# Kernel tuning notes

Measured on AMD Instinct MI355X. Metric: run time of the kernel, lower is better.

## Reference

```python
import jax, jax.numpy as jnp
import numpy as np

N = 100000   # nodes
E = 1600000  # edges
F_IN = 4
H = 64
G = 1000     # graphs in batch
C = 3        # num_classes
L = 2        # num_unit (LEConv layers)


def setup_inputs() -> dict:
    key = jax.random.key(0)
    ks = jax.random.split(key, 14)
    s = 0.1
    return {
        "x": jax.random.normal(ks[0], (N, F_IN), jnp.float32),
        "edge_index": jax.random.randint(ks[1], (2, E), 0, N, dtype=jnp.int32),
        "edge_attr": jax.random.uniform(ks[2], (E,), jnp.float32),
        "batch": jnp.sort(jax.random.randint(ks[3], (N,), 0, G, dtype=jnp.int32)),
        "w_emb": jax.random.normal(ks[4], (F_IN, H), jnp.float32) * s,
        "b_emb": jnp.zeros((H,), jnp.float32),
        "lin1_w": jax.random.normal(ks[5], (L, H, H), jnp.float32) * s,
        "lin1_b": jnp.zeros((L, H), jnp.float32),
        "lin2_w": jax.random.normal(ks[6], (L, H, H), jnp.float32) * s,  # bias=False in PyG LEConv
        "lin3_w": jax.random.normal(ks[7], (L, H, H), jnp.float32) * s,
        "lin3_b": jnp.zeros((L, H), jnp.float32),
        "mlp_w1": jax.random.normal(ks[8], (H, 2 * H), jnp.float32) * s,
        "mlp_b1": jnp.zeros((2 * H,), jnp.float32),
        "mlp_w2": jax.random.normal(ks[9], (2 * H, C), jnp.float32) * s,
        "mlp_b2": jnp.zeros((C,), jnp.float32),
    }


def reference(x, edge_index, edge_attr, batch, w_emb, b_emb,
              lin1_w, lin1_b, lin2_w, lin3_w, lin3_b,
              mlp_w1, mlp_b1, mlp_w2, mlp_b2):
    src, dst = edge_index[0], edge_index[1]  # message flows src(j) -> dst(i)
    h = x @ w_emb + b_emb  # [N, H]
    for l in range(L):
        a = h @ lin1_w[l] + lin1_b[l]            # lin1(x_j) source side
        b = h @ lin2_w[l]                         # lin2(x_i) target side, no bias
        msg = (a[src] - b[dst]) * edge_attr[:, None]   # [E, H]
        agg = jax.ops.segment_sum(msg, dst, num_segments=N)
        h = jax.nn.relu(agg + h @ lin3_w[l] + lin3_b[l])
    # global_mean_pool
    sums = jax.ops.segment_sum(h, batch, num_segments=G)        # [G, H]
    counts = jax.ops.segment_sum(jnp.ones((N,), h.dtype), batch, num_segments=G)
    graph_x = sums / jnp.maximum(counts, 1.0)[:, None]
    # causal_mlp head
    return jax.nn.relu(graph_x @ mlp_w1 + mlp_b1) @ mlp_w2 + mlp_b2  # [G, C]
```

## Files before the change

### kernel.cpp

```cpp
#include <hip/hip_runtime.h>

#define N_NODES 100000
#define N_EDGES 1600000
#define F_INPUT 4
#define HDIM 64
#define G_GRAPHS 1000
#define C_CLS 3

#define NPB 256
#define BSHIFT 8
#define NB 391
#define CBLK 98
#define CSR_CAP 6144
#define HIST_BLOCKS 512
#define BNDS_BLOCKS 391

typedef __attribute__((ext_vector_type(8))) short bf16x8;
typedef __attribute__((ext_vector_type(4))) float f32x4;

__device__ __forceinline__ unsigned short f2bf(float f) {
    unsigned u = __float_as_uint(f);
    unsigned r = (u + 0x7FFF + ((u >> 16) & 1)) >> 16;
    return (unsigned short)r;
}
__device__ __forceinline__ float bflo(unsigned u) {
    return __uint_as_float(u << 16);
}
__device__ __forceinline__ float bfhi(unsigned u) {
    return __uint_as_float(u & 0xFFFF0000u);
}
__device__ __forceinline__ float bf1(unsigned short s) {
    return __uint_as_float(((unsigned)s) << 16);
}

__global__ __launch_bounds__(256) void k_prew(
    const float* __restrict__ w_emb, const float* __restrict__ b_emb,
    const float* __restrict__ lin1_w, const float* __restrict__ lin1_b,
    const float* __restrict__ lin2_w,
    const float* __restrict__ lin3_w, const float* __restrict__ lin3_b,
    float* __restrict__ wp, float* __restrict__ bp, int* __restrict__ bcnt) {
    int t = threadIdx.x;
    for (int i = t; i < NB; i += 256) bcnt[i] = 0;
    int k = t >> 6, f = t & 63;
    const float* Ws[3] = {lin1_w, lin2_w, lin3_w};
#pragma unroll
    for (int m = 0; m < 3; ++m) {
        float s = 0.f;
        for (int j = 0; j < HDIM; ++j) s += w_emb[k * HDIM + j] * Ws[m][j * HDIM + f];
        wp[m * 256 + k * HDIM + f] = s;
    }
    if (t < HDIM) {
#pragma unroll
        for (int m = 0; m < 3; ++m) {
            float s = 0.f;
            for (int j = 0; j < HDIM; ++j) s += b_emb[j] * Ws[m][j * HDIM + t];
            if (m == 0) s += lin1_b[t];
            if (m == 2) s += lin3_b[t];
            bp[m * HDIM + t] = s;
        }
    }
}

__global__ __launch_bounds__(256) void k_hist_bounds(
    const int* __restrict__ dst, int* __restrict__ bcnt,
    const int* __restrict__ batch, int* __restrict__ goff) {
    __shared__ int s[NB];
    if (blockIdx.x < HIST_BLOCKS) {
        int bb = blockIdx.x;
        for (int i = threadIdx.x; i < NB; i += 256) s[i] = 0;
        __syncthreads();
        const int4* dst4 = (const int4*)dst;
        for (int e4 = bb * 256 + threadIdx.x; e4 < N_EDGES / 4; e4 += HIST_BLOCKS * 256) {
            int4 d = dst4[e4];
            atomicAdd(&s[d.x >> BSHIFT], 1);
            atomicAdd(&s[d.y >> BSHIFT], 1);
            atomicAdd(&s[d.z >> BSHIFT], 1);
            atomicAdd(&s[d.w >> BSHIFT], 1);
        }
        __syncthreads();
        for (int i = threadIdx.x; i < NB; i += 256)
            if (s[i]) atomicAdd(&bcnt[i], s[i]);
    } else {
        int n = (blockIdx.x - HIST_BLOCKS) * 256 + threadIdx.x;
        if (n >= N_NODES) return;
        int bv = batch[n];
        int bp_ = (n == 0) ? -1 : batch[n - 1];
        for (int g = bp_ + 1; g <= bv; ++g) goff[g] = n;
        if (n == N_NODES - 1) {
            for (int g = bv + 1; g <= G_GRAPHS; ++g) goff[g] = N_NODES;
        }
    }
}

__global__ __launch_bounds__(512) void k_boff(
    const int* __restrict__ bcnt, int* __restrict__ boff, int* __restrict__ bcur) {
    __shared__ int s[512];
    int t = threadIdx.x;
    int v = (t < NB) ? bcnt[t] : 0;
    s[t] = v;
    __syncthreads();
    for (int d = 1; d < 512; d <<= 1) {
        int x2 = (t >= d) ? s[t - d] : 0;
        __syncthreads();
        s[t] += x2;
        __syncthreads();
    }
    int ex = s[t] - v;
    if (t < NB) { boff[t] = ex; bcur[t] = ex; }
    if (t == 0) boff[NB] = N_EDGES;
}

__global__ __launch_bounds__(1024) void k_bucket(const int* __restrict__ src,
                                                 const int* __restrict__ dst,
                                                 const float* __restrict__ attr,
                                                 int* __restrict__ bcur,
                                                 int2* __restrict__ bbuf) {
    __shared__ int cnt[NB];
    __shared__ int base[NB];
    for (int i = threadIdx.x; i < NB; i += 1024) cnt[i] = 0;
    __syncthreads();
    int e0 = blockIdx.x * 16384;
    int myb[16], myrank[16];
    int2 mypack[16];
#pragma unroll
    for (int k = 0; k < 16; ++k) {
        int e = e0 + k * 1024 + threadIdx.x;
        if (e < N_EDGES) {
            int d = dst[e];
            int b = d >> BSHIFT;
            myb[k] = b;
            myrank[k] = atomicAdd(&cnt[b], 1);
            mypack[k].x = src[e] | ((d & (NPB - 1)) << 17);
            mypack[k].y = __float_as_int(attr[e]);
        } else
            myb[k] = -1;
    }
    __syncthreads();
    for (int i = threadIdx.x; i < NB; i += 1024)
        base[i] = cnt[i] ? atomicAdd(&bcur[i], cnt[i]) : 0;
    __syncthreads();
#pragma unroll
    for (int k = 0; k < 16; ++k)
        if (myb[k] >= 0) bbuf[base[myb[k]] + myrank[k]] = mypack[k];
}

__global__ __launch_bounds__(256) void k_csr(const int2* __restrict__ bbuf,
                                             const int* __restrict__ boff,
                                             int* __restrict__ off,
                                             float* __restrict__ wsum,
                                             int2* __restrict__ edge2) {
    __shared__ int2 se[CSR_CAP];
    __shared__ int deg[NPB];
    __shared__ float wsm[NPB];
    __shared__ int loff[NPB];
    __shared__ int sct[256];
    int b = blockIdx.x;
    int lo = boff[b];
    int cnt = boff[b + 1] - lo;
    if (cnt > CSR_CAP) cnt = CSR_CAP;
    int t = threadIdx.x;
    deg[t] = 0;
    wsm[t] = 0.f;
    for (int i = t; i < cnt; i += 256) se[i] = bbuf[lo + i];
    __syncthreads();
    for (int i = t; i < cnt; i += 256) {
        int2 p = se[i];
        int dloc = (p.x >> 17) & (NPB - 1);
        atomicAdd(&deg[dloc], 1);
        atomicAdd(&wsm[dloc], __int_as_float(p.y));
    }
    __syncthreads();
    int v = deg[t];
    sct[t] = v;
    __syncthreads();
    for (int d = 1; d < 256; d <<= 1) {
        int x2 = (t >= d) ? sct[t - d] : 0;
        __syncthreads();
        sct[t] += x2;
        __syncthreads();
    }
    int ex = sct[t] - v;
    loff[t] = ex;
    __syncthreads();
    int n = b * NPB + t;
    if (n < N_NODES) { off[n] = lo + ex; wsum[n] = wsm[t]; }
    if (b == NB - 1 && t == 0) off[N_NODES] = N_EDGES;
    deg[t] = 0;
    __syncthreads();
    for (int i = t; i < cnt; i += 256) {
        int2 p = se[i];
        int dloc = (p.x >> 17) & (NPB - 1);
        int r = atomicAdd(&deg[dloc], 1);
        edge2[lo + loff[dloc] + r] = make_int2(p.x & 0x1FFFF, p.y);
    }
}

__global__ __launch_bounds__(256) void k_gemm1st(
    const float* __restrict__ x, const float* __restrict__ wp,
    const float* __restrict__ bp, const float* __restrict__ wsum,
    unsigned short* __restrict__ a_out, unsigned short* __restrict__ d_out_) {
    int wave = threadIdx.x >> 6;
    int lane = threadIdx.x & 63;
    int row = lane & 15;
    int kg = lane >> 4;
    int base = blockIdx.x * 64;
    int col = wave * 16 + row;

    bf16x8 Bf[3];
#pragma unroll
    for (int m = 0; m < 3; ++m) {
        union { bf16x8 v; unsigned short u[8]; } fr;
#pragma unroll
        for (int j = 0; j < 8; ++j)
            fr.u[j] = (kg == 0 && j < F_INPUT) ? f2bf(wp[m * 256 + j * HDIM + col])
                                               : (unsigned short)0;
        Bf[m] = fr.v;
    }
    float bias1 = bp[col], bias2 = bp[HDIM + col], bias3 = bp[2 * HDIM + col];

    f32x4 acc[3][4];
#pragma unroll
    for (int m = 0; m < 3; ++m)
#pragma unroll
        for (int t = 0; t < 4; ++t) acc[m][t] = (f32x4){0.f, 0.f, 0.f, 0.f};

#pragma unroll
    for (int t = 0; t < 4; ++t) {
        int n = base + t * 16 + row;
        union { bf16x8 v; unsigned short u[8]; } af;
#pragma unroll
        for (int j = 0; j < 8; ++j) af.u[j] = 0;
        if (kg == 0 && n < N_NODES) {
            float4 xv = *(const float4*)(x + (size_t)n * F_INPUT);
            af.u[0] = f2bf(xv.x); af.u[1] = f2bf(xv.y);
            af.u[2] = f2bf(xv.z); af.u[3] = f2bf(xv.w);
        }
#pragma unroll
        for (int m = 0; m < 3; ++m)
            acc[m][t] = __builtin_amdgcn_mfma_f32_16x16x32_bf16(af.v, Bf[m], acc[m][t], 0, 0, 0);
    }

#pragma unroll
    for (int t = 0; t < 4; ++t) {
#pragma unroll
        for (int r = 0; r < 4; ++r) {
            int n = base + t * 16 + kg * 4 + r;
            if (n >= N_NODES) continue;
            float ws = wsum[n];
            float av = acc[0][t][r] + bias1;
            float dv = acc[2][t][r] + bias3 - (acc[1][t][r] + bias2) * ws;
            a_out[(size_t)n * HDIM + col] = f2bf(av);
            d_out_[(size_t)n * HDIM + col] = f2bf(dv);
        }
    }
}

__global__ __launch_bounds__(256) void k_gemm3(
    const unsigned short* __restrict__ h,
    const float* __restrict__ W1, const float* __restrict__ b1,
    const float* __restrict__ W2,
    const float* __restrict__ W3, const float* __restrict__ b3,
    const float* __restrict__ wsum,
    unsigned short* __restrict__ a_out, unsigned short* __restrict__ d_out_) {
    int wave = threadIdx.x >> 6;
    int lane = threadIdx.x & 63;
    int row = lane & 15;
    int kg = lane >> 4;
    int base = blockIdx.x * 64;
    int col = wave * 16 + row;

    bf16x8 Bf[3][2];
    const float* Ws[3] = {W1, W2, W3};
#pragma unroll
    for (int m = 0; m < 3; ++m)
#pragma unroll
        for (int hf = 0; hf < 2; ++hf) {
            union { bf16x8 v; unsigned short u[8]; } fr;
#pragma unroll
            for (int j = 0; j < 8; ++j) {
                int k = hf * 32 + kg * 8 + j;
                fr.u[j] = f2bf(Ws[m][k * HDIM + col]);
            }
            Bf[m][hf] = fr.v;
        }

    float bias1 = b1[col];
    float bias3 = b3[col];

    f32x4 acc[3][4];
#pragma unroll
    for (int m = 0; m < 3; ++m)
#pragma unroll
        for (int t = 0; t < 4; ++t) acc[m][t] = (f32x4){0.f, 0.f, 0.f, 0.f};

#pragma unroll
    for (int t = 0; t < 4; ++t) {
        int n = base + t * 16 + row;
        bf16x8 a0, a1;
        if (n < N_NODES) {
            const unsigned short* hr = h + (size_t)n * HDIM;
            a0 = *(const bf16x8*)(hr + kg * 8);
            a1 = *(const bf16x8*)(hr + 32 + kg * 8);
        } else {
            a0 = (bf16x8){0,0,0,0,0,0,0,0};
            a1 = (bf16x8){0,0,0,0,0,0,0,0};
        }
#pragma unroll
        for (int m = 0; m < 3; ++m) {
            acc[m][t] = __builtin_amdgcn_mfma_f32_16x16x32_bf16(a0, Bf[m][0], acc[m][t], 0, 0, 0);
            acc[m][t] = __builtin_amdgcn_mfma_f32_16x16x32_bf16(a1, Bf[m][1], acc[m][t], 0, 0, 0);
        }
    }

#pragma unroll
    for (int t = 0; t < 4; ++t) {
#pragma unroll
        for (int r = 0; r < 4; ++r) {
            int n = base + t * 16 + kg * 4 + r;
            if (n >= N_NODES) continue;
            float ws = wsum[n];
            float av = acc[0][t][r] + bias1;
            float dv = acc[2][t][r] + bias3 - acc[1][t][r] * ws;
            a_out[(size_t)n * HDIM + col] = f2bf(av);
            d_out_[(size_t)n * HDIM + col] = f2bf(dv);
        }
    }
}

__global__ __launch_bounds__(256) void k_agg(const int2* __restrict__ edge2,
                                             const int* __restrict__ off,
                                             const unsigned short* __restrict__ a,
                                             const unsigned short* __restrict__ dbuf,
                                             unsigned short* __restrict__ h) {
    int wid = threadIdx.x >> 6;
    int lane = threadIdx.x & 63;
    int slot = lane >> 3;
    int fo = lane & 7;
    int n = blockIdx.x * 4 + wid;
    if (n >= N_NODES) return;
    int lo = off[n], hi = off[n + 1];

    float acc[8];
#pragma unroll
    for (int q = 0; q < 8; ++q) acc[q] = 0.f;

#define GATHER_ADD(J)                                                        \
    if ((J) < hi) {                                                          \
        int2 p = edge2[(J)];                                                 \
        float w = __int_as_float(p.y);                                       \
        uint4 u = *(const uint4*)(a + (size_t)p.x * HDIM + fo * 8);          \
        acc[0] += bflo(u.x) * w; acc[1] += bfhi(u.x) * w;                    \
        acc[2] += bflo(u.y) * w; acc[3] += bfhi(u.y) * w;                    \
        acc[4] += bflo(u.z) * w; acc[5] += bfhi(u.z) * w;                    \
        acc[6] += bflo(u.w) * w; acc[7] += bfhi(u.w) * w;                    \
    }

    for (int j0 = lo; j0 < hi; j0 += 32) {
        GATHER_ADD(j0 + slot)
        GATHER_ADD(j0 + 8 + slot)
        GATHER_ADD(j0 + 16 + slot)
        GATHER_ADD(j0 + 24 + slot)
    }
#undef GATHER_ADD

#pragma unroll
    for (int m = 8; m <= 32; m <<= 1) {
#pragma unroll
        for (int q = 0; q < 8; ++q) acc[q] += __shfl_xor(acc[q], m);
    }

    if (slot == 0) {
        size_t o = (size_t)n * HDIM + fo * 8;
        uint4 dv = *(const uint4*)(dbuf + o);
        float dd[8] = {bflo(dv.x), bfhi(dv.x), bflo(dv.y), bfhi(dv.y),
                       bflo(dv.z), bfhi(dv.z), bflo(dv.w), bfhi(dv.w)};
        unsigned r[4];
#pragma unroll
        for (int q = 0; q < 4; ++q) {
            unsigned lo16 = f2bf(fmaxf(acc[2 * q] + dd[2 * q], 0.f));
            unsigned hi16 = f2bf(fmaxf(acc[2 * q + 1] + dd[2 * q + 1], 0.f));
            r[q] = lo16 | (hi16 << 16);
        }
        *(uint4*)(h + o) = make_uint4(r[0], r[1], r[2], r[3]);
    }
}

__global__ __launch_bounds__(256) void k_poolhead(const unsigned short* __restrict__ h,
                                                  const int* __restrict__ goff,
                                                  const float* __restrict__ W1,
                                                  const float* __restrict__ b1,
                                                  const float* __restrict__ W2,
                                                  const float* __restrict__ b2,
                                                  float* __restrict__ out) {
    int g = blockIdx.x;
    __shared__ float part[256];
    __shared__ float sx[HDIM];
    __shared__ float sy[2 * HDIM];
    int t = threadIdx.x;
    int lo = goff[g], hi = goff[g + 1];
    int f = t & 63, quarter = t >> 6;
    float acc = 0.f;
    for (int n = lo + quarter; n < hi; n += 4) acc += bf1(h[(size_t)n * HDIM + f]);
    part[t] = acc;
    __syncthreads();
    if (t < HDIM)
        sx[t] = (part[t] + part[t + 64] + part[t + 128] + part[t + 192]) /
                fmaxf((float)(hi - lo), 1.f);
    __syncthreads();
    if (t < 2 * HDIM) {
        float a1 = b1[t];
        for (int k = 0; k < HDIM; ++k) a1 += sx[k] * W1[k * 2 * HDIM + t];
        sy[t] = fmaxf(a1, 0.f);
    }
    __syncthreads();
    if (t < C_CLS) {
        float o = b2[t];
        for (int k = 0; k < 2 * HDIM; ++k) o += sy[k] * W2[k * C_CLS + t];
        out[g * C_CLS + t] = o;
    }
}

extern "C" void kernel_launch(void* const* d_in, const int* in_sizes, int n_in,
                              void* d_out, int out_size, void* d_ws, size_t ws_size,
                              hipStream_t stream) {
    const float* x      = (const float*)d_in[0];
    const int*   ei     = (const int*)d_in[1];
    const float* eattr  = (const float*)d_in[2];
    const int*   batch  = (const int*)d_in[3];
    const float* w_emb  = (const float*)d_in[4];
    const float* b_emb  = (const float*)d_in[5];
    const float* lin1_w = (const float*)d_in[6];
    const float* lin1_b = (const float*)d_in[7];
    const float* lin2_w = (const float*)d_in[8];
    const float* lin3_w = (const float*)d_in[9];
    const float* lin3_b = (const float*)d_in[10];
    const float* mlp_w1 = (const float*)d_in[11];
    const float* mlp_b1 = (const float*)d_in[12];
    const float* mlp_w2 = (const float*)d_in[13];
    const float* mlp_b2 = (const float*)d_in[14];
    float* out = (float*)d_out;

    const int* src = ei;
    const int* dst = ei + N_EDGES;

    const size_t NH = (size_t)N_NODES * HDIM;
    unsigned short* abf = (unsigned short*)d_ws;
    unsigned short* dbf = abf + NH;
    unsigned short* h   = dbf + NH;
    float* wsum = (float*)(h + NH);
    int2* edge2 = (int2*)(wsum + N_NODES);
    int2* bbuf  = edge2 + N_EDGES;
    int* off    = (int*)(bbuf + N_EDGES);
    int* bcnt   = off + N_NODES + 1;
    int* bcur   = bcnt + NB;
    int* boff   = bcur + NB;
    int* goff   = boff + NB + 1;
    float* wp   = (float*)(goff + G_GRAPHS + 1);
    float* bp   = wp + 3 * 256;

    k_prew<<<1, 256, 0, stream>>>(w_emb, b_emb,
                                  lin1_w, lin1_b, lin2_w, lin3_w, lin3_b, wp, bp, bcnt);
    k_hist_bounds<<<HIST_BLOCKS + BNDS_BLOCKS, 256, 0, stream>>>(dst, bcnt, batch, goff);
    k_boff<<<1, 512, 0, stream>>>(bcnt, boff, bcur);
    k_bucket<<<CBLK, 1024, 0, stream>>>(src, dst, eattr, bcur, bbuf);
    k_csr<<<NB, 256, 0, stream>>>(bbuf, boff, off, wsum, edge2);

    int gemm_blocks = (N_NODES + 63) / 64;
    int agg_blocks = (N_NODES + 3) / 4;

    k_gemm1st<<<gemm_blocks, 256, 0, stream>>>(x, wp, bp, wsum, abf, dbf);
    k_agg<<<agg_blocks, 256, 0, stream>>>(edge2, off, abf, dbf, h);
    k_gemm3<<<gemm_blocks, 256, 0, stream>>>(h, lin1_w + HDIM * HDIM, lin1_b + HDIM,
                                             lin2_w + HDIM * HDIM,
                                             lin3_w + HDIM * HDIM, lin3_b + HDIM,
                                             wsum, abf, dbf);
    k_agg<<<agg_blocks, 256, 0, stream>>>(edge2, off, abf, dbf, h);
    k_poolhead<<<G_GRAPHS, 256, 0, stream>>>(h, goff, mlp_w1, mlp_b1, mlp_w2, mlp_b2, out);
}
```

Measured before the change: 228.2 us.

## Store node features in 8-column slabs and pack edges into one 32-bit word

Node feature buffers (a, d, h) are changed from row-major [N,64] to eight slabs of [N,8], so each aggregation block gathers only from one 1.6 MB slab, which is meant to raise cache hit rates on the random source gathers. Edge records shrink from int2 to a single 32-bit word: a 17-bit source index plus the edge weight quantised to 15 bits, halving edge-stream traffic. The aggregation kernel is rewritten so each block handles one feature slab and 16 nodes, with 16 lanes per node, at the cost of reading the edge list eight times. The 15-bit weight quantisation adds numerical error.

Measured after the change: 289.0 us. +26.6%, slower.

```diff
diff --git a/kernel.cpp b/kernel.cpp
--- a/kernel.cpp
+++ b/kernel.cpp
@@ -14,6 +14,9 @@
 #define CSR_CAP 6144
 #define HIST_BLOCKS 512
 #define BNDS_BLOCKS 391
+#define AGGT_BLOCKS 50000
+
+#define N8 ((size_t)N_NODES * 8)
 
 typedef __attribute__((ext_vector_type(8))) short bf16x8;
 typedef __attribute__((ext_vector_type(4))) float f32x4;
@@ -148,7 +151,7 @@
                                              const int* __restrict__ boff,
                                              int* __restrict__ off,
                                              float* __restrict__ wsum,
-                                             int2* __restrict__ edge2) {
+                                             unsigned* __restrict__ edge1) {
     __shared__ int2 se[CSR_CAP];
     __shared__ int deg[NPB];
     __shared__ float wsm[NPB];
@@ -191,14 +194,15 @@
         int2 p = se[i];
         int dloc = (p.x >> 17) & (NPB - 1);
         int r = atomicAdd(&deg[dloc], 1);
-        edge2[lo + loff[dloc] + r] = make_int2(p.x & 0x1FFFF, p.y);
+        unsigned w15 = (unsigned)(__int_as_float(p.y) * 32767.f + 0.5f);
+        edge1[lo + loff[dloc] + r] = ((unsigned)p.x & 0x1FFFFu) | (w15 << 17);
     }
 }
 
 __global__ __launch_bounds__(256) void k_gemm1st(
     const float* __restrict__ x, const float* __restrict__ wp,
     const float* __restrict__ bp, const float* __restrict__ wsum,
-    unsigned short* __restrict__ a_out, unsigned short* __restrict__ d_out_) {
+    unsigned short* __restrict__ a_t, unsigned short* __restrict__ d_t) {
     int wave = threadIdx.x >> 6;
     int lane = threadIdx.x & 63;
     int row = lane & 15;
@@ -240,6 +244,7 @@
             acc[m][t] = __builtin_amdgcn_mfma_f32_16x16x32_bf16(af.v, Bf[m], acc[m][t], 0, 0, 0);
     }
 
+    size_t tbase = (size_t)(col >> 3) * N8 + (col & 7);
 #pragma unroll
     for (int t = 0; t < 4; ++t) {
 #pragma unroll
@@ -249,19 +254,19 @@
             float ws = wsum[n];
             float av = acc[0][t][r] + bias1;
             float dv = acc[2][t][r] + bias3 - (acc[1][t][r] + bias2) * ws;
-            a_out[(size_t)n * HDIM + col] = f2bf(av);
-            d_out_[(size_t)n * HDIM + col] = f2bf(dv);
+            a_t[tbase + (size_t)n * 8] = f2bf(av);
+            d_t[tbase + (size_t)n * 8] = f2bf(dv);
         }
     }
 }
 
 __global__ __launch_bounds__(256) void k_gemm3(
-    const unsigned short* __restrict__ h,
+    const unsigned short* __restrict__ h_t,
     const float* __restrict__ W1, const float* __restrict__ b1,
     const float* __restrict__ W2,
     const float* __restrict__ W3, const float* __restrict__ b3,
     const float* __restrict__ wsum,
-    unsigned short* __restrict__ a_out, unsigned short* __restrict__ d_out_) {
+    unsigned short* __restrict__ a_t, unsigned short* __restrict__ d_t) {
     int wave = threadIdx.x >> 6;
     int lane = threadIdx.x & 63;
     int row = lane & 15;
@@ -298,9 +303,8 @@
         int n = base + t * 16 + row;
         bf16x8 a0, a1;
         if (n < N_NODES) {
-            const unsigned short* hr = h + (size_t)n * HDIM;
-            a0 = *(const bf16x8*)(hr + kg * 8);
-            a1 = *(const bf16x8*)(hr + 32 + kg * 8);
+            a0 = *(const bf16x8*)(h_t + (size_t)kg * N8 + (size_t)n * 8);
+            a1 = *(const bf16x8*)(h_t + (size_t)(kg + 4) * N8 + (size_t)n * 8);
         } else {
             a0 = (bf16x8){0,0,0,0,0,0,0,0};
             a1 = (bf16x8){0,0,0,0,0,0,0,0};
@@ -312,6 +316,7 @@
         }
     }
 
+    size_t tbase = (size_t)(col >> 3) * N8 + (col & 7);
 #pragma unroll
     for (int t = 0; t < 4; ++t) {
 #pragma unroll
@@ -321,57 +326,48 @@
             float ws = wsum[n];
             float av = acc[0][t][r] + bias1;
             float dv = acc[2][t][r] + bias3 - acc[1][t][r] * ws;
-            a_out[(size_t)n * HDIM + col] = f2bf(av);
-            d_out_[(size_t)n * HDIM + col] = f2bf(dv);
-        }
-    }
-}
-
-__global__ __launch_bounds__(256) void k_agg(const int2* __restrict__ edge2,
-                                             const int* __restrict__ off,
-                                             const unsigned short* __restrict__ a,
-                                             const unsigned short* __restrict__ dbuf,
-                                             unsigned short* __restrict__ h) {
-    int wid = threadIdx.x >> 6;
-    int lane = threadIdx.x & 63;
-    int slot = lane >> 3;
-    int fo = lane & 7;
-    int n = blockIdx.x * 4 + wid;
-    if (n >= N_NODES) return;
+            a_t[tbase + (size_t)n * 8] = f2bf(av);
+            d_t[tbase + (size_t)n * 8] = f2bf(dv);
+        }
+    }
+}
+
+__global__ __launch_bounds__(256) void k_agg_t(const unsigned* __restrict__ edge1,
+                                               const int* __restrict__ off,
+                                               const unsigned short* __restrict__ a_t,
+                                               const unsigned short* __restrict__ d_t,
+                                               unsigned short* __restrict__ h_t) {
+    int fo = blockIdx.x & 7;
+    int grp = blockIdx.x >> 3;
+    int wid = threadIdx.x >> 6, lane = threadIdx.x & 63;
+    int slot = lane >> 4, el = lane & 15;
+    int n = grp * 16 + wid * 4 + slot;
     int lo = off[n], hi = off[n + 1];
+    const unsigned short* abase = a_t + (size_t)fo * N8;
 
     float acc[8];
 #pragma unroll
     for (int q = 0; q < 8; ++q) acc[q] = 0.f;
 
-#define GATHER_ADD(J)                                                        \
-    if ((J) < hi) {                                                          \
-        int2 p = edge2[(J)];                                                 \
-        float w = __int_as_float(p.y);                                       \
-        uint4 u = *(const uint4*)(a + (size_t)p.x * HDIM + fo * 8);          \
-        acc[0] += bflo(u.x) * w; acc[1] += bfhi(u.x) * w;                    \
-        acc[2] += bflo(u.y) * w; acc[3] += bfhi(u.y) * w;                    \
-        acc[4] += bflo(u.z) * w; acc[5] += bfhi(u.z) * w;                    \
-        acc[6] += bflo(u.w) * w; acc[7] += bfhi(u.w) * w;                    \
-    }
-
-    for (int j0 = lo; j0 < hi; j0 += 32) {
-        GATHER_ADD(j0 + slot)
-        GATHER_ADD(j0 + 8 + slot)
-        GATHER_ADD(j0 + 16 + slot)
-        GATHER_ADD(j0 + 24 + slot)
-    }
-#undef GATHER_ADD
-
-#pragma unroll
-    for (int m = 8; m <= 32; m <<= 1) {
+    for (int j = lo + el; j < hi; j += 16) {
+        unsigned p = edge1[j];
+        float w = (float)(p >> 17) * (1.0f / 32767.0f);
+        uint4 u = *(const uint4*)(abase + (size_t)(p & 0x1FFFFu) * 8);
+        acc[0] += bflo(u.x) * w; acc[1] += bfhi(u.x) * w;
+        acc[2] += bflo(u.y) * w; acc[3] += bfhi(u.y) * w;
+        acc[4] += bflo(u.z) * w; acc[5] += bfhi(u.z) * w;
+        acc[6] += bflo(u.w) * w; acc[7] += bfhi(u.w) * w;
+    }
+
+#pragma unroll
+    for (int m = 1; m <= 8; m <<= 1) {
 #pragma unroll
         for (int q = 0; q < 8; ++q) acc[q] += __shfl_xor(acc[q], m);
     }
 
-    if (slot == 0) {
-        size_t o = (size_t)n * HDIM + fo * 8;
-        uint4 dv = *(const uint4*)(dbuf + o);
+    if (el == 0) {
+        size_t o = (size_t)fo * N8 + (size_t)n * 8;
+        uint4 dv = *(const uint4*)(d_t + o);
         float dd[8] = {bflo(dv.x), bfhi(dv.x), bflo(dv.y), bfhi(dv.y),
                        bflo(dv.z), bfhi(dv.z), bflo(dv.w), bfhi(dv.w)};
         unsigned r[4];
@@ -381,11 +377,11 @@
             unsigned hi16 = f2bf(fmaxf(acc[2 * q + 1] + dd[2 * q + 1], 0.f));
             r[q] = lo16 | (hi16 << 16);
         }
-        *(uint4*)(h + o) = make_uint4(r[0], r[1], r[2], r[3]);
-    }
-}
-
-__global__ __launch_bounds__(256) void k_poolhead(const unsigned short* __restrict__ h,
+        *(uint4*)(h_t + o) = make_uint4(r[0], r[1], r[2], r[3]);
+    }
+}
+
+__global__ __launch_bounds__(256) void k_poolhead(const unsigned short* __restrict__ h_t,
                                                   const int* __restrict__ goff,
                                                   const float* __restrict__ W1,
                                                   const float* __restrict__ b1,
@@ -399,8 +395,9 @@
     int t = threadIdx.x;
     int lo = goff[g], hi = goff[g + 1];
     int f = t & 63, quarter = t >> 6;
+    size_t fb = (size_t)(f >> 3) * N8 + (f & 7);
     float acc = 0.f;
-    for (int n = lo + quarter; n < hi; n += 4) acc += bf1(h[(size_t)n * HDIM + f]);
+    for (int n = lo + quarter; n < hi; n += 4) acc += bf1(h_t[fb + (size_t)n * 8]);
     part[t] = acc;
     __syncthreads();
     if (t < HDIM)
@@ -448,8 +445,8 @@
     unsigned short* dbf = abf + NH;
     unsigned short* h   = dbf + NH;
     float* wsum = (float*)(h + NH);
-    int2* edge2 = (int2*)(wsum + N_NODES);
-    int2* bbuf  = edge2 + N_EDGES;
+    unsigned* edge1 = (unsigned*)(wsum + N_NODES);
+    int2* bbuf  = (int2*)(edge1 + N_EDGES);
     int* off    = (int*)(bbuf + N_EDGES);
     int* bcnt   = off + N_NODES + 1;
     int* bcur   = bcnt + NB;
@@ -463,17 +460,16 @@
     k_hist_bounds<<<HIST_BLOCKS + BNDS_BLOCKS, 256, 0, stream>>>(dst, bcnt, batch, goff);
     k_boff<<<1, 512, 0, stream>>>(bcnt, boff, bcur);
     k_bucket<<<CBLK, 1024, 0, stream>>>(src, dst, eattr, bcur, bbuf);
-    k_csr<<<NB, 256, 0, stream>>>(bbuf, boff, off, wsum, edge2);
+    k_csr<<<NB, 256, 0, stream>>>(bbuf, boff, off, wsum, edge1);
 
     int gemm_blocks = (N_NODES + 63) / 64;
-    int agg_blocks = (N_NODES + 3) / 4;
 
     k_gemm1st<<<gemm_blocks, 256, 0, stream>>>(x, wp, bp, wsum, abf, dbf);
-    k_agg<<<agg_blocks, 256, 0, stream>>>(edge2, off, abf, dbf, h);
+    k_agg_t<<<AGGT_BLOCKS, 256, 0, stream>>>(edge1, off, abf, dbf, h);
     k_gemm3<<<gemm_blocks, 256, 0, stream>>>(h, lin1_w + HDIM * HDIM, lin1_b + HDIM,
                                              lin2_w + HDIM * HDIM,
                                              lin3_w + HDIM * HDIM, lin3_b + HDIM,
                                              wsum, abf, dbf);
-    k_agg<<<agg_blocks, 256, 0, stream>>>(edge2, off, abf, dbf, h);
+    k_agg_t<<<AGGT_BLOCKS, 256, 0, stream>>>(edge1, off, abf, dbf, h);
     k_poolhead<<<G_GRAPHS, 256, 0, stream>>>(h, goff, mlp_w1, mlp_b1, mlp_w2, mlp_b2, out);
 }
```
